# Kernel tuning notes

Measured on AMD Instinct MI355X. Metric: run time of the kernel, lower is better.

## Reference

```python
import jax, jax.numpy as jnp
import numpy as np

DIMS = 64        # channel dim of the block (== num_heads, forced by the module's asserts)
HEADS = 64       # per-head channels c = DIMS // HEADS = 1
B, H, W = 2, 16, DIMS  # residual add requires spatial width == DIMS


def _conv1x1(t, Wt, bt):
    # 1x1 Conv2d == channel-mixing GEMM
    return jnp.einsum('oc,bchw->bohw', Wt, t) + bt[None, :, None, None]


def setup_inputs() -> dict:
    key = jax.random.key(0)
    ks = jax.random.split(key, 9)
    sc = 1.0 / np.sqrt(DIMS)
    inp = {'x': jax.random.normal(ks[0], (B, DIMS, H, W), jnp.float32)}
    names = [('Wq', 'bq'), ('Wk', 'bk'), ('Wv', 'bv'), ('Wo', 'bo')]
    for i, (wn, bn) in enumerate(names):
        inp[wn] = jax.random.normal(ks[1 + 2 * i], (DIMS, DIMS), jnp.float32) * sc
        inp[bn] = jax.random.normal(ks[2 + 2 * i], (DIMS,), jnp.float32) * 0.01
    return inp


def reference(x, Wq, bq, Wk, bk, Wv, bv, Wo, bo):
    b, C, h, w = x.shape
    g = HEADS
    c = C // g            # per-head channels (== 1 here)
    S = h * w             # spatial sequence length
    # QKV projections (1x1 convs), split heads: (b, g*c, h, w) -> (b*g, c, S)
    q = _conv1x1(x, Wq, bq).reshape(b * g, c, S)
    k = _conv1x1(x, Wk, bk).reshape(b * g, c, S)
    v = _conv1x1(x, Wv, bv).reshape(b * g, c, S)
    # attention over spatial positions; scale is 1/sqrt(dims) per the source
    scores = jnp.einsum('bcs,bct->bst', q, k) / (DIMS ** 0.5)
    attn = jax.nn.softmax(scores, axis=-1)   # dropout is identity in eval mode
    o = jnp.einsum('bst,bct->bcs', attn, v)  # (b*g, c, S)
    # rearrange '(b g) s (h w) -> b (g s) h w' with w=DIMS (faithful to source)
    o = o.reshape(b, g * c, S // DIMS, DIMS)
    return x + _conv1x1(o, Wo, bo)
```

## Files before the change

kernel.cpp:

```cpp
#include <hip/hip_runtime.h>

#define BB     2
#define CC     64
#define SS     1024
#define PSC    (0.125f * 1.44269504f)
#define PI_F   3.14159265358979f
#define NCHEB  16
#define CSTRIDE 34
#define STILE  16
#define MAGIC  0x5F3C2B1Au

#if __has_builtin(__builtin_amdgcn_exp2f)
#define EXP2(x) __builtin_amdgcn_exp2f(x)
#else
#define EXP2(x) exp2f(x)
#endif

__global__ __launch_bounds__(1024) void fused_attn_kernel(
    const float* __restrict__ x,
    const float* __restrict__ Wq, const float* __restrict__ bq,
    const float* __restrict__ Wk, const float* __restrict__ bk,
    const float* __restrict__ Wv, const float* __restrict__ bv,
    const float* __restrict__ Wo, const float* __restrict__ bo,
    float* __restrict__ out, float* __restrict__ ws)
{
    unsigned* flags  = (unsigned*)ws;
    float*    coeffs = ws + 128;

    const int tid  = threadIdx.x;
    const int lane = tid & 63;
    const int wv   = tid >> 6;

    __shared__ union {
        struct {
            float ks[SS], vs[SS];
            float wred[16];
            float Fse[NCHEB], Fsv[NCHEB];
        } p;
        struct {
            float xs[CC][STILE];
            float cofs[CC * CSTRIDE];
            float Os[CC][STILE];
        } c;
    } sm;

    if (blockIdx.x < 128) {
        const int head = blockIdx.x;
        const int b    = head >> 6;
        const int o    = head & 63;

        const float* __restrict__ wqp = Wq + o * CC;
        const float* __restrict__ wkp = Wk + o * CC;
        const float* __restrict__ wvp = Wv + o * CC;
        const float* __restrict__ xb  = x + b * CC * SS + tid;

        float qa = bq[o], ka = bk[o], va = bv[o];
        #pragma unroll 16
        for (int c = 0; c < CC; ++c) {
            const float xv = xb[c * SS];
            qa = fmaf(wqp[c], xv, qa);
            ka = fmaf(wkp[c], xv, ka);
            va = fmaf(wvp[c], xv, va);
        }
        sm.p.ks[tid] = ka;
        sm.p.vs[tid] = va;
        const float p = qa * PSC;

        float am = fabsf(p);
        #pragma unroll
        for (int off = 32; off; off >>= 1)
            am = fmaxf(am, __shfl_xor(am, off, 64));
        if (lane == 0) sm.p.wred[wv] = am;
        __syncthreads();

        float pmax = sm.p.wred[0];
        #pragma unroll
        for (int i = 1; i < 16; ++i) pmax = fmaxf(pmax, sm.p.wred[i]);
        pmax = fmaxf(pmax, 1e-20f);

        const float pj = pmax * __cosf((2 * wv + 1) * (PI_F / (2 * NCHEB)));
        float se = 0.f, sv = 0.f;
        #pragma unroll
        for (int i = 0; i < 16; ++i) {
            const int t = lane + 64 * i;
            const float e = EXP2(pj * sm.p.ks[t]);
            se += e;
            sv = fmaf(e, sm.p.vs[t], sv);
        }
        #pragma unroll
        for (int off = 32; off; off >>= 1) {
            se += __shfl_xor(se, off, 64);
            sv += __shfl_xor(sv, off, 64);
        }
        if (lane == 0) { sm.p.Fse[wv] = se; sm.p.Fsv[wv] = sv; }
        __syncthreads();

        float* __restrict__ C = coeffs + head * CSTRIDE;
        if (tid < 2 * NCHEB) {
            const int  n  = tid & (NCHEB - 1);
            const bool fn = tid >= NCHEB;
            const float* __restrict__ F = fn ? sm.p.Fsv : sm.p.Fse;
            float acc = 0.f;
            #pragma unroll
            for (int j = 0; j < NCHEB; ++j)
                acc = fmaf(F[j], __cosf(n * (2 * j + 1) * (PI_F / (2 * NCHEB))), acc);
            acc *= (n == 0) ? (1.f / NCHEB) : (2.f / NCHEB);
            __hip_atomic_store(C + (fn ? NCHEB : 0) + n, acc,
                               __ATOMIC_RELAXED, __HIP_MEMORY_SCOPE_AGENT);
        }
        if (tid == 0)
            __hip_atomic_store(C + 32, pmax,
                               __ATOMIC_RELAXED, __HIP_MEMORY_SCOPE_AGENT);
        __syncthreads();
        if (tid == 0)
            __hip_atomic_store(&flags[head], MAGIC,
                               __ATOMIC_RELEASE, __HIP_MEMORY_SCOPE_AGENT);
    } else {
        const int cid = blockIdx.x - 128;
        const int b   = cid >> 6;
        const int s0  = (cid & 63) * STILE;
        const int o   = tid >> 4;
        const int si  = tid & 15;

        sm.c.xs[o][si] = x[(b * CC + o) * SS + s0 + si];
        __syncthreads();

        const float* __restrict__ wqo = Wq + o * CC;
        float q = bq[o];
        #pragma unroll 16
        for (int c = 0; c < CC; ++c)
            q = fmaf(wqo[c], sm.c.xs[c][si], q);

        if (tid < 64) {
            while (__hip_atomic_load(&flags[b * 64 + tid],
                                     __ATOMIC_ACQUIRE, __HIP_MEMORY_SCOPE_AGENT)
                   != MAGIC)
                __builtin_amdgcn_s_sleep(2);
        }
        __syncthreads();

        const float* __restrict__ gc = coeffs + b * 64 * CSTRIDE;
        for (int i = tid; i < 64 * CSTRIDE; i += 1024)
            sm.c.cofs[i] = __hip_atomic_load(gc + i,
                                             __ATOMIC_RELAXED, __HIP_MEMORY_SCOPE_AGENT);
        __syncthreads();

        const float* __restrict__ Ch = sm.c.cofs + o * CSTRIDE;
        const float pmax = Ch[32];
        const float u  = q * PSC / pmax;
        const float tu = 2.f * u;
        float b1 = 0.f, b2 = 0.f, d1 = 0.f, d2 = 0.f;
        #pragma unroll
        for (int n = NCHEB - 1; n >= 1; --n) {
            const float nb = fmaf(tu, b1, Ch[n] - b2);
            b2 = b1; b1 = nb;
            const float nd = fmaf(tu, d1, Ch[NCHEB + n] - d2);
            d2 = d1; d1 = nd;
        }
        const float fse = fmaf(u, b1, Ch[0] - b2);
        const float fsv = fmaf(u, d1, Ch[NCHEB] - d2);
        sm.c.Os[o][si] = fsv / fse;
        __syncthreads();

        const float* __restrict__ woo = Wo + o * CC;
        float acc = bo[o];
        #pragma unroll 16
        for (int c = 0; c < CC; ++c)
            acc = fmaf(woo[c], sm.c.Os[c][si], acc);
        out[(b * CC + o) * SS + s0 + si] = sm.c.xs[o][si] + acc;
    }
}

extern "C" void kernel_launch(void* const* d_in, const int* in_sizes, int n_in,
                              void* d_out, int out_size, void* d_ws, size_t ws_size,
                              hipStream_t stream) {
    const float* x  = (const float*)d_in[0];
    const float* Wq = (const float*)d_in[1];
    const float* bq = (const float*)d_in[2];
    const float* Wk = (const float*)d_in[3];
    const float* bk = (const float*)d_in[4];
    const float* Wv = (const float*)d_in[5];
    const float* bv = (const float*)d_in[6];
    const float* Wo = (const float*)d_in[7];
    const float* bo = (const float*)d_in[8];
    float* out = (float*)d_out;
    float* ws  = (float*)d_ws;

    fused_attn_kernel<<<256, 1024, 0, stream>>>(x, Wq, bq, Wk, bk, Wv, bv,
                                                Wo, bo, out, ws);
}
```

Baseline: 89.17 us.

## Split fused flag-synchronized kernel into two sequential launches

Replaces the single kernel, where evaluation blocks spin-wait on per-head global flags set by coefficient blocks, with two kernels launched in order on the stream. The stream ordering provides the dependency, so the atomic flags, sleeps and acquire loads go away. It adds one kernel launch boundary but removes the inter-block spin and any dependence on co-residency or stale flag state.

After: 81.65 us. -8.4%, faster.

```diff
diff --git a/kernel.cpp b/kernel.cpp
--- a/kernel.cpp
+++ b/kernel.cpp
@@ -1,6 +1,5 @@
 #include <hip/hip_runtime.h>
 
-#define BB     2
 #define CC     64
 #define SS     1024
 #define PSC    (0.125f * 1.44269504f)
@@ -8,7 +7,6 @@
 #define NCHEB  16
 #define CSTRIDE 34
 #define STILE  16
-#define MAGIC  0x5F3C2B1Au
 
 #if __has_builtin(__builtin_amdgcn_exp2f)
 #define EXP2(x) __builtin_amdgcn_exp2f(x)
@@ -16,159 +14,138 @@
 #define EXP2(x) exp2f(x)
 #endif
 
-__global__ __launch_bounds__(1024) void fused_attn_kernel(
+__global__ __launch_bounds__(1024) void coeff_kernel(
     const float* __restrict__ x,
     const float* __restrict__ Wq, const float* __restrict__ bq,
     const float* __restrict__ Wk, const float* __restrict__ bk,
     const float* __restrict__ Wv, const float* __restrict__ bv,
-    const float* __restrict__ Wo, const float* __restrict__ bo,
-    float* __restrict__ out, float* __restrict__ ws)
+    float* __restrict__ coeffs)
 {
-    unsigned* flags  = (unsigned*)ws;
-    float*    coeffs = ws + 128;
-
+    const int head = blockIdx.x;
+    const int b    = head >> 6;
+    const int o    = head & 63;
     const int tid  = threadIdx.x;
     const int lane = tid & 63;
     const int wv   = tid >> 6;
 
-    __shared__ union {
-        struct {
-            float ks[SS], vs[SS];
-            float wred[16];
-            float Fse[NCHEB], Fsv[NCHEB];
-        } p;
-        struct {
-            float xs[CC][STILE];
-            float cofs[CC * CSTRIDE];
-            float Os[CC][STILE];
-        } c;
-    } sm;
+    __shared__ float ks[SS], vs[SS];
+    __shared__ float wred[16];
+    __shared__ float Fse[NCHEB], Fsv[NCHEB];
 
-    if (blockIdx.x < 128) {
-        const int head = blockIdx.x;
-        const int b    = head >> 6;
-        const int o    = head & 63;
+    const float* __restrict__ wqp = Wq + o * CC;
+    const float* __restrict__ wkp = Wk + o * CC;
+    const float* __restrict__ wvp = Wv + o * CC;
+    const float* __restrict__ xb  = x + b * CC * SS + tid;
 
-        const float* __restrict__ wqp = Wq + o * CC;
-        const float* __restrict__ wkp = Wk + o * CC;
-        const float* __restrict__ wvp = Wv + o * CC;
-        const float* __restrict__ xb  = x + b * CC * SS + tid;
+    float qa = bq[o], ka = bk[o], va = bv[o];
+    #pragma unroll 16
+    for (int c = 0; c < CC; ++c) {
+        const float xv = xb[c * SS];
+        qa = fmaf(wqp[c], xv, qa);
+        ka = fmaf(wkp[c], xv, ka);
+        va = fmaf(wvp[c], xv, va);
+    }
+    ks[tid] = ka;
+    vs[tid] = va;
+    const float p = qa * PSC;
 
-        float qa = bq[o], ka = bk[o], va = bv[o];
-        #pragma unroll 16
-        for (int c = 0; c < CC; ++c) {
-            const float xv = xb[c * SS];
-            qa = fmaf(wqp[c], xv, qa);
-            ka = fmaf(wkp[c], xv, ka);
-            va = fmaf(wvp[c], xv, va);
-        }
-        sm.p.ks[tid] = ka;
-        sm.p.vs[tid] = va;
-        const float p = qa * PSC;
+    float am = fabsf(p);
+    #pragma unroll
+    for (int off = 32; off; off >>= 1)
+        am = fmaxf(am, __shfl_xor(am, off, 64));
+    if (lane == 0) wred[wv] = am;
+    __syncthreads();
 
-        float am = fabsf(p);
+    float pmax = wred[0];
+    #pragma unroll
+    for (int i = 1; i < 16; ++i) pmax = fmaxf(pmax, wred[i]);
+    pmax = fmaxf(pmax, 1e-20f);
+
+    const float pj = pmax * __cosf((2 * wv + 1) * (PI_F / (2 * NCHEB)));
+    float se = 0.f, sv = 0.f;
+    #pragma unroll
+    for (int i = 0; i < 16; ++i) {
+        const int t = lane + 64 * i;
+        const float e = EXP2(pj * ks[t]);
+        se += e;
+        sv = fmaf(e, vs[t], sv);
+    }
+    #pragma unroll
+    for (int off = 32; off; off >>= 1) {
+        se += __shfl_xor(se, off, 64);
+        sv += __shfl_xor(sv, off, 64);
+    }
+    if (lane == 0) { Fse[wv] = se; Fsv[wv] = sv; }
+    __syncthreads();
+
+    float* __restrict__ C = coeffs + head * CSTRIDE;
+    if (tid < 2 * NCHEB) {
+        const int  n  = tid & (NCHEB - 1);
+        const bool fn = tid >= NCHEB;
+        const float* __restrict__ F = fn ? Fsv : Fse;
+        float acc = 0.f;
         #pragma unroll
-        for (int off = 32; off; off >>= 1)
-            am = fmaxf(am, __shfl_xor(am, off, 64));
-        if (lane == 0) sm.p.wred[wv] = am;
-        __syncthreads();
+        for (int j = 0; j < NCHEB; ++j)
+            acc = fmaf(F[j], __cosf(n * (2 * j + 1) * (PI_F / (2 * NCHEB))), acc);
+        acc *= (n == 0) ? (1.f / NCHEB) : (2.f / NCHEB);
+        C[(fn ? NCHEB : 0) + n] = acc;
+    }
+    if (tid == 0) C[32] = pmax;
+}
 
-        float pmax = sm.p.wred[0];
-        #pragma unroll
-        for (int i = 1; i < 16; ++i) pmax = fmaxf(pmax, sm.p.wred[i]);
-        pmax = fmaxf(pmax, 1e-20f);
+__global__ __launch_bounds__(1024) void eval_kernel(
+    const float* __restrict__ x,
+    const float* __restrict__ Wq, const float* __restrict__ bq,
+    const float* __restrict__ Wo, const float* __restrict__ bo,
+    const float* __restrict__ coeffs,
+    float* __restrict__ out)
+{
+    const int cid = blockIdx.x;
+    const int b   = cid >> 6;
+    const int s0  = (cid & 63) * STILE;
+    const int tid = threadIdx.x;
+    const int o   = tid >> 4;
+    const int si  = tid & 15;
 
-        const float pj = pmax * __cosf((2 * wv + 1) * (PI_F / (2 * NCHEB)));
-        float se = 0.f, sv = 0.f;
-        #pragma unroll
-        for (int i = 0; i < 16; ++i) {
-            const int t = lane + 64 * i;
-            const float e = EXP2(pj * sm.p.ks[t]);
-            se += e;
-            sv = fmaf(e, sm.p.vs[t], sv);
-        }
-        #pragma unroll
-        for (int off = 32; off; off >>= 1) {
-            se += __shfl_xor(se, off, 64);
-            sv += __shfl_xor(sv, off, 64);
-        }
-        if (lane == 0) { sm.p.Fse[wv] = se; sm.p.Fsv[wv] = sv; }
-        __syncthreads();
+    __shared__ float xs[CC][STILE];
+    __shared__ float cofs[CC * CSTRIDE];
+    __shared__ float Os[CC][STILE];
 
-        float* __restrict__ C = coeffs + head * CSTRIDE;
-        if (tid < 2 * NCHEB) {
-            const int  n  = tid & (NCHEB - 1);
-            const bool fn = tid >= NCHEB;
-            const float* __restrict__ F = fn ? sm.p.Fsv : sm.p.Fse;
-            float acc = 0.f;
-            #pragma unroll
-            for (int j = 0; j < NCHEB; ++j)
-                acc = fmaf(F[j], __cosf(n * (2 * j + 1) * (PI_F / (2 * NCHEB))), acc);
-            acc *= (n == 0) ? (1.f / NCHEB) : (2.f / NCHEB);
-            __hip_atomic_store(C + (fn ? NCHEB : 0) + n, acc,
-                               __ATOMIC_RELAXED, __HIP_MEMORY_SCOPE_AGENT);
-        }
-        if (tid == 0)
-            __hip_atomic_store(C + 32, pmax,
-                               __ATOMIC_RELAXED, __HIP_MEMORY_SCOPE_AGENT);
-        __syncthreads();
-        if (tid == 0)
-            __hip_atomic_store(&flags[head], MAGIC,
-                               __ATOMIC_RELEASE, __HIP_MEMORY_SCOPE_AGENT);
-    } else {
-        const int cid = blockIdx.x - 128;
-        const int b   = cid >> 6;
-        const int s0  = (cid & 63) * STILE;
-        const int o   = tid >> 4;
-        const int si  = tid & 15;
+    xs[o][si] = x[(b * CC + o) * SS + s0 + si];
+    const float* __restrict__ gc = coeffs + b * CC * CSTRIDE;
+    for (int i = tid; i < CC * CSTRIDE; i += 1024)
+        cofs[i] = gc[i];
+    __syncthreads();
 
-        sm.c.xs[o][si] = x[(b * CC + o) * SS + s0 + si];
-        __syncthreads();
+    const float* __restrict__ wqo = Wq + o * CC;
+    float q = bq[o];
+    #pragma unroll 16
+    for (int c = 0; c < CC; ++c)
+        q = fmaf(wqo[c], xs[c][si], q);
 
-        const float* __restrict__ wqo = Wq + o * CC;
-        float q = bq[o];
-        #pragma unroll 16
-        for (int c = 0; c < CC; ++c)
-            q = fmaf(wqo[c], sm.c.xs[c][si], q);
+    const float* __restrict__ Ch = cofs + o * CSTRIDE;
+    const float pmax = Ch[32];
+    const float u  = q * PSC / pmax;
+    const float tu = 2.f * u;
+    float b1 = 0.f, b2 = 0.f, d1 = 0.f, d2 = 0.f;
+    #pragma unroll
+    for (int n = NCHEB - 1; n >= 1; --n) {
+        const float nb = fmaf(tu, b1, Ch[n] - b2);
+        b2 = b1; b1 = nb;
+        const float nd = fmaf(tu, d1, Ch[NCHEB + n] - d2);
+        d2 = d1; d1 = nd;
+    }
+    const float fse = fmaf(u, b1, Ch[0] - b2);
+    const float fsv = fmaf(u, d1, Ch[NCHEB] - d2);
+    Os[o][si] = fsv / fse;
+    __syncthreads();
 
-        if (tid < 64) {
-            while (__hip_atomic_load(&flags[b * 64 + tid],
-                                     __ATOMIC_ACQUIRE, __HIP_MEMORY_SCOPE_AGENT)
-                   != MAGIC)
-                __builtin_amdgcn_s_sleep(2);
-        }
-        __syncthreads();
-
-        const float* __restrict__ gc = coeffs + b * 64 * CSTRIDE;
-        for (int i = tid; i < 64 * CSTRIDE; i += 1024)
-            sm.c.cofs[i] = __hip_atomic_load(gc + i,
-                                             __ATOMIC_RELAXED, __HIP_MEMORY_SCOPE_AGENT);
-        __syncthreads();
-
-        const float* __restrict__ Ch = sm.c.cofs + o * CSTRIDE;
-        const float pmax = Ch[32];
-        const float u  = q * PSC / pmax;
-        const float tu = 2.f * u;
-        float b1 = 0.f, b2 = 0.f, d1 = 0.f, d2 = 0.f;
-        #pragma unroll
-        for (int n = NCHEB - 1; n >= 1; --n) {
-            const float nb = fmaf(tu, b1, Ch[n] - b2);
-            b2 = b1; b1 = nb;
-            const float nd = fmaf(tu, d1, Ch[NCHEB + n] - d2);
-            d2 = d1; d1 = nd;
-        }
-        const float fse = fmaf(u, b1, Ch[0] - b2);
-        const float fsv = fmaf(u, d1, Ch[NCHEB] - d2);
-        sm.c.Os[o][si] = fsv / fse;
-        __syncthreads();
-
-        const float* __restrict__ woo = Wo + o * CC;
-        float acc = bo[o];
-        #pragma unroll 16
-        for (int c = 0; c < CC; ++c)
-            acc = fmaf(woo[c], sm.c.Os[c][si], acc);
-        out[(b * CC + o) * SS + s0 + si] = sm.c.xs[o][si] + acc;
-    }
+    const float* __restrict__ woo = Wo + o * CC;
+    float acc = bo[o];
+    #pragma unroll 16
+    for (int c = 0; c < CC; ++c)
+        acc = fmaf(woo[c], Os[c][si], acc);
+    out[(b * CC + o) * SS + s0 + si] = xs[o][si] + acc;
 }
 
 extern "C" void kernel_launch(void* const* d_in, const int* in_sizes, int n_in,
@@ -184,8 +161,9 @@
     const float* Wo = (const float*)d_in[7];
     const float* bo = (const float*)d_in[8];
     float* out = (float*)d_out;
-    float* ws  = (float*)d_ws;
 
-    fused_attn_kernel<<<256, 1024, 0, stream>>>(x, Wq, bq, Wk, bk, Wv, bv,
-                                                Wo, bo, out, ws);
+    float* coeffs = (float*)d_ws;
+
+    coeff_kernel<<<128, 1024, 0, stream>>>(x, Wq, bq, Wk, bk, Wv, bv, coeffs);
+    eval_kernel <<<128, 1024, 0, stream>>>(x, Wq, bq, Wo, bo, coeffs, out);
 }
```
